# Optimization experiments

Hardware: AMD Instinct MI355X
Metric: run time of the kernel (lower is better)

Reference implementation:

```python
import jax, jax.numpy as jnp
import numpy as np

GROUP_SIZE = 7
ROI_SCALE = 1.3
BIN_SCALE = 1.5


def setup_inputs() -> dict:
    key = jax.random.key(0)
    k1, k2, k3, k4 = jax.random.split(key, 4)
    B, C, H, W = 2, 490, 128, 128  # C = output_dim(10) * group_size(7)**2
    N = 512
    stride = 16
    features = jax.random.normal(k1, (B, C, H, W), dtype=jnp.float32)
    img_w = W * stride
    bidx = jax.random.randint(k2, (N, 1), 0, B).astype(jnp.float32)
    xy1 = jax.random.uniform(k3, (N, 2), minval=0.0, maxval=img_w - 64.0)
    wh = jax.random.uniform(k4, (N, 2), minval=32.0, maxval=512.0)
    xy2 = jnp.minimum(xy1 + wh, img_w - 1.0)
    rois = jnp.concatenate([bidx, xy1[:, 0:1], xy1[:, 1:2], xy2[:, 0:1], xy2[:, 1:2]], axis=1)
    return {"rois": rois, "features": features, "stride": stride}


def reference(rois, features, stride):
    G = GROUP_SIZE
    B, C, H, W = features.shape
    D = C // (G * G)  # output_dim, computed dynamically as in the torch module
    dt = features.dtype
    spatial_scale = 1.0 / stride

    rois = rois[:, :5].astype(dt)
    batch_idx = rois[:, 0].astype(jnp.int32)  # [N]
    # rounded roi corners in feature-map coordinates (end is inclusive +1)
    rsw = jnp.round(rois[:, 1]) * spatial_scale
    rsh = jnp.round(rois[:, 2]) * spatial_scale
    rew = (jnp.round(rois[:, 3]) + 1.0) * spatial_scale
    reh = (jnp.round(rois[:, 4]) + 1.0) * spatial_scale
    # mask (context) enlargement around roi center by ROI_SCALE
    rw, rh = rew - rsw, reh - rsh
    rwm, rhm = rw * ROI_SCALE, rh * ROI_SCALE
    swm = (rsw + rew) * 0.5 - rwm * 0.5
    shm = (rsh + reh) * 0.5 - rhm * 0.5
    rwm = jnp.maximum(rwm, 0.1)  # force tiny rois to 1x1
    rhm = jnp.maximum(rhm, 0.1)
    bin_h = rhm / G  # [N]
    bin_w = rwm / G
    dh = bin_h * (BIN_SCALE - 1.0) * 0.5  # extra bin context
    dw = bin_w * (BIN_SCALE - 1.0) * 0.5

    g = jnp.arange(G, dtype=dt)  # bin index
    hstart = jnp.clip(jnp.floor(shm[:, None] + g[None, :] * bin_h[:, None] - dh[:, None]), 0, H).astype(jnp.int32)  # [N,G]
    hend = jnp.clip(jnp.ceil(shm[:, None] + (g[None, :] + 1.0) * bin_h[:, None] + dh[:, None]), 0, H).astype(jnp.int32)
    wstart = jnp.clip(jnp.floor(swm[:, None] + g[None, :] * bin_w[:, None] - dw[:, None]), 0, W).astype(jnp.int32)
    wend = jnp.clip(jnp.ceil(swm[:, None] + (g[None, :] + 1.0) * bin_w[:, None] + dw[:, None]), 0, W).astype(jnp.int32)

    # integral image so each bin-average is 4 gathers instead of a dynamic loop
    cs = jnp.cumsum(jnp.cumsum(features, axis=2), axis=3)
    S = jnp.pad(cs, ((0, 0), (0, 0), (1, 0), (1, 0)))  # [B,C,H+1,W+1]
    # position-sensitive channel map c = (d*G + ph)*G + pw  <=>  reshape C -> [D,G,G]
    Sr = S.reshape(B, D, G, G, H + 1, W + 1)

    N = rois.shape[0]
    b_ = batch_idx[:, None, None, None]          # [N,1,1,1]
    d_ = jnp.arange(D)[None, :, None, None]      # [1,D,1,1]
    pi = jnp.arange(G)[None, None, :, None]      # [1,1,G,1] (ph)
    pj = jnp.arange(G)[None, None, None, :]      # [1,1,1,G] (pw)
    hs = hstart[:, None, :, None]
    he = hend[:, None, :, None]
    ws = wstart[:, None, None, :]
    we = wend[:, None, None, :]

    total = (Sr[b_, d_, pi, pj, he, we] - Sr[b_, d_, pi, pj, hs, we]
             - Sr[b_, d_, pi, pj, he, ws] + Sr[b_, d_, pi, pj, hs, ws])  # [N,D,G,G]

    area = ((hend - hstart)[:, None, :, None] * (wend - wstart)[:, None, None, :])  # [N,1->D,G,G] via broadcast
    area = jnp.broadcast_to(area, total.shape)
    out = jnp.where(area > 0, total / jnp.maximum(area, 1).astype(dt), jnp.zeros((), dt))
    return out
```

## Files before the change

### kernel.cpp

```cpp
#include <hip/hip_runtime.h>

#define GS   7
#define CCH  490
#define HH   128
#define WW   128
#define LDW  132
#define NB   2
#define NCH  (NB * CCH)
#define NBLK 512

__global__ __launch_bounds__(512, 4) void psroi_fused(
    const float* __restrict__ rois,
    const float* __restrict__ feat,
    const int*   __restrict__ stride_p,
    float*       __restrict__ out)
{
#pragma clang fp contract(off)
    __shared__ float S[HH * LDW];

    const int tid = threadIdx.x;
    const int col = tid & 127;
    const int seg = tid >> 7;
    const int r0  = seg * 32;
    const int row = tid >> 2;
    const int ws_ = tid & 3;

    const float ss  = 1.0f / (float)(*stride_p);
    const float b_f = rois[tid * 5 + 0];
    const int   bi  = (int)b_f;
    const float x1  = rois[tid * 5 + 1];
    const float y1  = rois[tid * 5 + 2];
    const float x2  = rois[tid * 5 + 3];
    const float y2  = rois[tid * 5 + 4];
    float rsw = rintf(x1) * ss;
    float rsh = rintf(y1) * ss;
    float rew = (rintf(x2) + 1.0f) * ss;
    float reh = (rintf(y2) + 1.0f) * ss;
    float rwm = (rew - rsw) * 1.3f;
    float rhm = (reh - rsh) * 1.3f;
    const float swm = (rsw + rew) * 0.5f - rwm * 0.5f;
    const float shm = (rsh + reh) * 0.5f - rhm * 0.5f;
    rwm = fmaxf(rwm, 0.1f);
    rhm = fmaxf(rhm, 0.1f);
    const float bin_h = rhm / 7.0f;
    const float bin_w = rwm / 7.0f;
    const float dh = bin_h * 0.25f;
    const float dw = bin_w * 0.25f;

    int ch = blockIdx.x;
    float v[32];
    {
        const float* __restrict__ fp = feat + (size_t)ch * (HH * WW) + r0 * WW + col;
        #pragma unroll
        for (int i = 0; i < 32; ++i)
            v[i] = fp[i * WW];
    }

    while (ch < NCH) {
        const int nxt = ch + NBLK;

        float p[32];
        if (nxt < NCH) {
            const float* __restrict__ fp = feat + (size_t)nxt * (HH * WW) + r0 * WW + col;
            #pragma unroll
            for (int i = 0; i < 32; ++i)
                p[i] = fp[i * WW];
        }

        #pragma unroll
        for (int i = 1; i < 32; ++i)
            v[i] += v[i - 1];

        S[seg * LDW + col] = v[31];
        __syncthreads();
        float offA = 0.0f;
        if (seg > 0) offA += S[0 * LDW + col];
        if (seg > 1) offA += S[1 * LDW + col];
        if (seg > 2) offA += S[2 * LDW + col];
        __syncthreads();

        {
            float* sp = &S[r0 * LDW + col];
            #pragma unroll
            for (int i = 0; i < 32; ++i)
                sp[i * LDW] = v[i] + offA;
        }
        __syncthreads();

        {
            float* rp = &S[row * LDW + ws_ * 32];
            float u[32];
            #pragma unroll
            for (int i = 0; i < 8; ++i) {
                const float4 q = *(const float4*)&rp[i * 4];
                u[4 * i + 0] = q.x; u[4 * i + 1] = q.y;
                u[4 * i + 2] = q.z; u[4 * i + 3] = q.w;
            }
            #pragma unroll
            for (int i = 1; i < 32; ++i)
                u[i] += u[i - 1];

            const float tot = u[31];
            const float t1 = __shfl_up(tot, 1, 64);
            const float t2 = __shfl_up(tot, 2, 64);
            const float t3 = __shfl_up(tot, 3, 64);
            float offB = 0.0f;
            if (ws_ > 0) offB += t1;
            if (ws_ > 1) offB += t2;
            if (ws_ > 2) offB += t3;

            #pragma unroll
            for (int i = 0; i < 8; ++i) {
                float4 q;
                q.x = u[4 * i + 0] + offB; q.y = u[4 * i + 1] + offB;
                q.z = u[4 * i + 2] + offB; q.w = u[4 * i + 3] + offB;
                *(float4*)&rp[i * 4] = q;
            }
        }
        __syncthreads();

        {
            const int b = ch / CCH;
            const int c = ch - b * CCH;
            if (bi == b) {
                const int d   = c / (GS * GS);
                const int rem = c - d * (GS * GS);
                const int pi  = rem / GS;
                const int pj  = rem - pi * GS;
                const float gi = (float)pi;
                const float gj = (float)pj;

                const int hs  = (int)fminf(fmaxf(floorf(shm + gi * bin_h - dh),          0.0f), 128.0f);
                const int he  = (int)fminf(fmaxf(ceilf (shm + (gi + 1.0f) * bin_h + dh), 0.0f), 128.0f);
                const int ws2 = (int)fminf(fmaxf(floorf(swm + gj * bin_w - dw),          0.0f), 128.0f);
                const int we  = (int)fminf(fmaxf(ceilf (swm + (gj + 1.0f) * bin_w + dw), 0.0f), 128.0f);

                const int area = (he - hs) * (we - ws2);
                const float A  = (he > 0 && we  > 0) ? S[(he - 1) * LDW + (we  - 1)] : 0.0f;
                const float Bv = (hs > 0 && we  > 0) ? S[(hs - 1) * LDW + (we  - 1)] : 0.0f;
                const float Cv = (he > 0 && ws2 > 0) ? S[(he - 1) * LDW + (ws2 - 1)] : 0.0f;
                const float Dv = (hs > 0 && ws2 > 0) ? S[(hs - 1) * LDW + (ws2 - 1)] : 0.0f;
                const float total = ((A - Bv) - Cv) + Dv;
                out[(size_t)tid * CCH + c] = (area > 0) ? (total / (float)area) : 0.0f;
            }
        }
        __syncthreads();

        #pragma unroll
        for (int i = 0; i < 32; ++i)
            v[i] = p[i];
        ch = nxt;
    }
}

extern "C" void kernel_launch(void* const* d_in, const int* in_sizes, int n_in,
                              void* d_out, int out_size, void* d_ws, size_t ws_size,
                              hipStream_t stream)
{
    const float* rois     = (const float*)d_in[0];
    const float* feat     = (const float*)d_in[1];
    const int*   stride_p = (const int*)d_in[2];
    float*       out      = (float*)d_out;

    dim3 grid(NBLK);
    dim3 block(512);
    hipLaunchKernelGGL(psroi_fused, grid, block, 0, stream, rois, feat, stride_p, out);
}
```

Before: 100.4 us.

## Split each channel's integral image across two half-height blocks and combine with atomics

Replaces the persistent 512-block loop, which prefetched the next channel into registers, with one block per (channel, half-height) pair, giving 1960 blocks. Each block builds a 64-row integral image in shared memory, so the shared-memory footprint halves and more blocks can be resident. Each ROI bin's partial box sum from each half is accumulated into the output with atomicAdd, which requires a memset of the output before the launch. In exchange it adds atomic traffic, an extra memset operation, and a floating-point summation order that differs from the original.

```diff
diff --git a/kernel.cpp b/kernel.cpp
--- a/kernel.cpp
+++ b/kernel.cpp
@@ -1,155 +1,144 @@
 #include <hip/hip_runtime.h>
 
-#define GS   7
-#define CCH  490
-#define HH   128
-#define WW   128
-#define LDW  132
-#define NB   2
-#define NCH  (NB * CCH)
-#define NBLK 512
+#define GS    7
+#define CCH   490
+#define HH    128
+#define HHF   64
+#define WW    128
+#define LDW   132
+#define NB    2
+#define NCH   (NB * CCH)
+#define NOUT  (512 * CCH)
 
-__global__ __launch_bounds__(512, 4) void psroi_fused(
+__global__ __launch_bounds__(512, 8) void psroi_half(
     const float* __restrict__ rois,
     const float* __restrict__ feat,
     const int*   __restrict__ stride_p,
     float*       __restrict__ out)
 {
 #pragma clang fp contract(off)
-    __shared__ float S[HH * LDW];
+    __shared__ float S[HHF * LDW];
+    __shared__ float T[4 * 128];
 
+    const int ch = blockIdx.x >> 1;
+    const int h  = blockIdx.x & 1;
     const int tid = threadIdx.x;
-    const int col = tid & 127;
-    const int seg = tid >> 7;
-    const int r0  = seg * 32;
-    const int row = tid >> 2;
-    const int ws_ = tid & 3;
 
-    const float ss  = 1.0f / (float)(*stride_p);
-    const float b_f = rois[tid * 5 + 0];
-    const int   bi  = (int)b_f;
-    const float x1  = rois[tid * 5 + 1];
-    const float y1  = rois[tid * 5 + 2];
-    const float x2  = rois[tid * 5 + 3];
-    const float y2  = rois[tid * 5 + 4];
-    float rsw = rintf(x1) * ss;
-    float rsh = rintf(y1) * ss;
-    float rew = (rintf(x2) + 1.0f) * ss;
-    float reh = (rintf(y2) + 1.0f) * ss;
-    float rwm = (rew - rsw) * 1.3f;
-    float rhm = (reh - rsh) * 1.3f;
-    const float swm = (rsw + rew) * 0.5f - rwm * 0.5f;
-    const float shm = (rsh + reh) * 0.5f - rhm * 0.5f;
-    rwm = fmaxf(rwm, 0.1f);
-    rhm = fmaxf(rhm, 0.1f);
-    const float bin_h = rhm / 7.0f;
-    const float bin_w = rwm / 7.0f;
-    const float dh = bin_h * 0.25f;
-    const float dw = bin_w * 0.25f;
+    {
+        const int col = tid & 127;
+        const int seg = tid >> 7;
+        const int r0  = seg * 16;
+        const float* __restrict__ fp =
+            feat + (size_t)ch * (HH * WW) + (h * HHF + r0) * WW + col;
 
-    int ch = blockIdx.x;
-    float v[32];
+        float v[16];
+        #pragma unroll
+        for (int i = 0; i < 16; ++i)
+            v[i] = fp[i * WW];
+        #pragma unroll
+        for (int i = 1; i < 16; ++i)
+            v[i] += v[i - 1];
+
+        T[seg * 128 + col] = v[15];
+        __syncthreads();
+        float offA = 0.0f;
+        if (seg > 0) offA += T[0 * 128 + col];
+        if (seg > 1) offA += T[1 * 128 + col];
+        if (seg > 2) offA += T[2 * 128 + col];
+
+        float* sp = &S[r0 * LDW + col];
+        #pragma unroll
+        for (int i = 0; i < 16; ++i)
+            sp[i * LDW] = v[i] + offA;
+    }
+    __syncthreads();
+
     {
-        const float* __restrict__ fp = feat + (size_t)ch * (HH * WW) + r0 * WW + col;
+        const int row = tid >> 3;
+        const int ws_ = tid & 7;
+        float* rp = &S[row * LDW + ws_ * 16];
+
+        float u[16];
         #pragma unroll
-        for (int i = 0; i < 32; ++i)
-            v[i] = fp[i * WW];
-    }
+        for (int i = 0; i < 4; ++i) {
+            const float4 q = *(const float4*)&rp[i * 4];
+            u[4 * i + 0] = q.x; u[4 * i + 1] = q.y;
+            u[4 * i + 2] = q.z; u[4 * i + 3] = q.w;
+        }
+        #pragma unroll
+        for (int i = 1; i < 16; ++i)
+            u[i] += u[i - 1];
 
-    while (ch < NCH) {
-        const int nxt = ch + NBLK;
-
-        float p[32];
-        if (nxt < NCH) {
-            const float* __restrict__ fp = feat + (size_t)nxt * (HH * WW) + r0 * WW + col;
-            #pragma unroll
-            for (int i = 0; i < 32; ++i)
-                p[i] = fp[i * WW];
-        }
+        float s = u[15];
+        float t;
+        t = __shfl_up(s, 1, 64); if ((tid & 7) >= 1) s += t;
+        t = __shfl_up(s, 2, 64); if ((tid & 7) >= 2) s += t;
+        t = __shfl_up(s, 4, 64); if ((tid & 7) >= 4) s += t;
+        float offB = __shfl_up(s, 1, 64);
+        if ((tid & 7) == 0) offB = 0.0f;
 
         #pragma unroll
-        for (int i = 1; i < 32; ++i)
-            v[i] += v[i - 1];
+        for (int i = 0; i < 4; ++i) {
+            float4 q;
+            q.x = u[4 * i + 0] + offB; q.y = u[4 * i + 1] + offB;
+            q.z = u[4 * i + 2] + offB; q.w = u[4 * i + 3] + offB;
+            *(float4*)&rp[i * 4] = q;
+        }
+    }
+    __syncthreads();
 
-        S[seg * LDW + col] = v[31];
-        __syncthreads();
-        float offA = 0.0f;
-        if (seg > 0) offA += S[0 * LDW + col];
-        if (seg > 1) offA += S[1 * LDW + col];
-        if (seg > 2) offA += S[2 * LDW + col];
-        __syncthreads();
+    {
+        const int n   = tid;
+        const int b   = ch / CCH;
+        const int c   = ch - b * CCH;
+        const int bi  = (int)rois[n * 5 + 0];
+        if (bi == b) {
+            const float ss = 1.0f / (float)(*stride_p);
+            const float x1 = rois[n * 5 + 1];
+            const float y1 = rois[n * 5 + 2];
+            const float x2 = rois[n * 5 + 3];
+            const float y2 = rois[n * 5 + 4];
 
-        {
-            float* sp = &S[r0 * LDW + col];
-            #pragma unroll
-            for (int i = 0; i < 32; ++i)
-                sp[i * LDW] = v[i] + offA;
-        }
-        __syncthreads();
+            float rsw = rintf(x1) * ss;
+            float rsh = rintf(y1) * ss;
+            float rew = (rintf(x2) + 1.0f) * ss;
+            float reh = (rintf(y2) + 1.0f) * ss;
+            float rwm = (rew - rsw) * 1.3f;
+            float rhm = (reh - rsh) * 1.3f;
+            const float swm = (rsw + rew) * 0.5f - rwm * 0.5f;
+            const float shm = (rsh + reh) * 0.5f - rhm * 0.5f;
+            rwm = fmaxf(rwm, 0.1f);
+            rhm = fmaxf(rhm, 0.1f);
+            const float bin_h = rhm / 7.0f;
+            const float bin_w = rwm / 7.0f;
+            const float dh = bin_h * 0.25f;
+            const float dw = bin_w * 0.25f;
 
-        {
-            float* rp = &S[row * LDW + ws_ * 32];
-            float u[32];
-            #pragma unroll
-            for (int i = 0; i < 8; ++i) {
-                const float4 q = *(const float4*)&rp[i * 4];
-                u[4 * i + 0] = q.x; u[4 * i + 1] = q.y;
-                u[4 * i + 2] = q.z; u[4 * i + 3] = q.w;
-            }
-            #pragma unroll
-            for (int i = 1; i < 32; ++i)
-                u[i] += u[i - 1];
+            const int d   = c / (GS * GS);
+            const int rem = c - d * (GS * GS);
+            const int pi  = rem / GS;
+            const int pj  = rem - pi * GS;
+            const float gi = (float)pi;
+            const float gj = (float)pj;
 
-            const float tot = u[31];
-            const float t1 = __shfl_up(tot, 1, 64);
-            const float t2 = __shfl_up(tot, 2, 64);
-            const float t3 = __shfl_up(tot, 3, 64);
-            float offB = 0.0f;
-            if (ws_ > 0) offB += t1;
-            if (ws_ > 1) offB += t2;
-            if (ws_ > 2) offB += t3;
+            const int hs  = (int)fminf(fmaxf(floorf(shm + gi * bin_h - dh),          0.0f), 128.0f);
+            const int he  = (int)fminf(fmaxf(ceilf (shm + (gi + 1.0f) * bin_h + dh), 0.0f), 128.0f);
+            const int ws2 = (int)fminf(fmaxf(floorf(swm + gj * bin_w - dw),          0.0f), 128.0f);
+            const int we  = (int)fminf(fmaxf(ceilf (swm + (gj + 1.0f) * bin_w + dw), 0.0f), 128.0f);
 
-            #pragma unroll
-            for (int i = 0; i < 8; ++i) {
-                float4 q;
-                q.x = u[4 * i + 0] + offB; q.y = u[4 * i + 1] + offB;
-                q.z = u[4 * i + 2] + offB; q.w = u[4 * i + 3] + offB;
-                *(float4*)&rp[i * 4] = q;
+            const int area = (he - hs) * (we - ws2);
+            const int ls = min(max(hs - h * HHF, 0), HHF);
+            const int le = min(max(he - h * HHF, 0), HHF);
+
+            if (area > 0 && le > ls && we > ws2) {
+                const float A  =              S[(le - 1) * LDW + (we  - 1)];
+                const float Bv = (ls  > 0) ?  S[(ls - 1) * LDW + (we  - 1)] : 0.0f;
+                const float Cv = (ws2 > 0) ?  S[(le - 1) * LDW + (ws2 - 1)] : 0.0f;
+                const float Dv = (ls > 0 && ws2 > 0) ? S[(ls - 1) * LDW + (ws2 - 1)] : 0.0f;
+                const float partial = ((A - Bv) - Cv) + Dv;
+                atomicAdd(&out[(size_t)n * CCH + c], partial / (float)area);
             }
         }
-        __syncthreads();
-
-        {
-            const int b = ch / CCH;
-            const int c = ch - b * CCH;
-            if (bi == b) {
-                const int d   = c / (GS * GS);
-                const int rem = c - d * (GS * GS);
-                const int pi  = rem / GS;
-                const int pj  = rem - pi * GS;
-                const float gi = (float)pi;
-                const float gj = (float)pj;
-
-                const int hs  = (int)fminf(fmaxf(floorf(shm + gi * bin_h - dh),          0.0f), 128.0f);
-                const int he  = (int)fminf(fmaxf(ceilf (shm + (gi + 1.0f) * bin_h + dh), 0.0f), 128.0f);
-                const int ws2 = (int)fminf(fmaxf(floorf(swm + gj * bin_w - dw),          0.0f), 128.0f);
-                const int we  = (int)fminf(fmaxf(ceilf (swm + (gj + 1.0f) * bin_w + dw), 0.0f), 128.0f);
-
-                const int area = (he - hs) * (we - ws2);
-                const float A  = (he > 0 && we  > 0) ? S[(he - 1) * LDW + (we  - 1)] : 0.0f;
-                const float Bv = (hs > 0 && we  > 0) ? S[(hs - 1) * LDW + (we  - 1)] : 0.0f;
-                const float Cv = (he > 0 && ws2 > 0) ? S[(he - 1) * LDW + (ws2 - 1)] : 0.0f;
-                const float Dv = (hs > 0 && ws2 > 0) ? S[(hs - 1) * LDW + (ws2 - 1)] : 0.0f;
-                const float total = ((A - Bv) - Cv) + Dv;
-                out[(size_t)tid * CCH + c] = (area > 0) ? (total / (float)area) : 0.0f;
-            }
-        }
-        __syncthreads();
-
-        #pragma unroll
-        for (int i = 0; i < 32; ++i)
-            v[i] = p[i];
-        ch = nxt;
     }
 }
 
@@ -162,7 +151,9 @@
     const int*   stride_p = (const int*)d_in[2];
     float*       out      = (float*)d_out;
 
-    dim3 grid(NBLK);
+    hipMemsetAsync(d_out, 0, (size_t)out_size * sizeof(float), stream);
+
+    dim3 grid(NCH * 2);
     dim3 block(512);
-    hipLaunchKernelGGL(psroi_fused, grid, block, 0, stream, rois, feat, stride_p, out);
+    hipLaunchKernelGGL(psroi_half, grid, block, 0, stream, rois, feat, stride_p, out);
 }
```

New measurement: 108.1 us. +7.7%, slower.
